# Kernel optimization log

Hardware: AMD Instinct MI355X
Metric: run time of the kernel (lower is better)

## Reference

```python
import jax, jax.numpy as jnp
import numpy as np

IN_H = IN_W = 128
OUT_H = OUT_W = 512
CHUNK = 65536  # = 256*256, same chunk size as the torch while-loop
EPS = 1e-6


def _conv3(x, w, b):
    y = jax.lax.conv_general_dilated(x, w, (1, 1), ((1, 1), (1, 1)),
                                     dimension_numbers=('NCHW', 'OIHW', 'NCHW'))
    return y + b[None, :, None, None]


def _centers(n):
    # torch.arange(-1,1,2/n)+1/n  ==  cell centers in (-1,1)
    return (jnp.arange(n, dtype=jnp.float32) + 0.5) * (2.0 / n) - 1.0


def setup_inputs() -> dict:
    key = jax.random.key(0)
    ks = iter(jax.random.split(key, 40))
    rnd = lambda shape, s: jax.random.normal(next(ks), shape, jnp.float32) * s
    inp = {
        'x': jax.random.uniform(next(ks), (1, 3, IN_H, IN_W), jnp.float32),
        'output_size': jnp.array([OUT_H, OUT_W], dtype=jnp.int32),
        # EDSR encoder params
        'head_w': rnd((64, 3, 3, 3), 0.05), 'head_b': rnd((64,), 0.01),
        'rb_w': rnd((16, 2, 64, 64, 3, 3), 0.02), 'rb_b': rnd((16, 2, 64), 0.01),
        'tail_w': rnd((64, 64, 3, 3), 0.02), 'tail_b': rnd((64,), 0.01),
        # MLP 580 -> 256 -> 256 -> 256 -> 256 -> 3
        'mw0': rnd((580, 256), 0.04), 'mb0': rnd((256,), 0.01),
        'mw1': rnd((256, 256), 0.06), 'mb1': rnd((256,), 0.01),
        'mw2': rnd((256, 256), 0.06), 'mb2': rnd((256,), 0.01),
        'mw3': rnd((256, 256), 0.06), 'mb3': rnd((256,), 0.01),
        'mw4': rnd((256, 3), 0.06), 'mb4': rnd((3,), 0.01),
    }
    return inp


def reference(x, output_size, head_w, head_b, rb_w, rb_b, tail_w, tail_b,
              mw0, mb0, mw1, mb1, mw2, mb2, mw3, mb3, mw4, mb4):
    # ---- EDSR encoder (head conv + 16 resblocks + tail conv, residual) ----
    h0 = _conv3(x, head_w, head_b)

    def block(h, wb):
        w0, b0, w1, b1 = wb
        return h + _conv3(jax.nn.relu(_conv3(h, w0, b0)), w1, b1), None

    hb, _ = jax.lax.scan(block, h0, (rb_w[:, 0], rb_b[:, 0], rb_w[:, 1], rb_b[:, 1]))
    feat64 = h0 + _conv3(hb, tail_w, tail_b)  # [1,64,H,W]
    B, C, H, W = feat64.shape

    # im2col 3x3 pad 1 -> channel order (c, kh, kw), matching torch im2col.view
    p = jnp.pad(feat64, ((0, 0), (0, 0), (1, 1), (1, 1)))
    feat = jnp.stack([p[:, :, i:i + H, j:j + W]
                      for i in range(3) for j in range(3)],
                     axis=2).reshape(B, C * 9, H, W)  # [1,576,H,W]

    # normalized cell-center coordinate map of the feature grid: [2,H,W], (h,w)
    fg = jnp.stack(jnp.meshgrid(_centers(H), _centers(W), indexing='ij'))

    ws = (mw0, mw1, mw2, mw3, mw4)
    bs = (mb0, mb1, mb2, mb3, mb4)

    def mlp(t):
        for w, b in zip(ws[:-1], bs[:-1]):
            t = jax.nn.relu(t @ w + b)
        return t @ ws[-1] + bs[-1]

    dh, dw = 1.0 / H, 1.0 / W
    hw = jnp.array([H, W], jnp.float32)
    q_cell = jnp.array([2.0 * H / OUT_H, 2.0 * W / OUT_W], jnp.float32)
    fimg = feat[0]  # [576,H,W]

    def sample(img, gh, gw):
        # torch grid_sampler nearest, align_corners=False, round-half-to-even
        iy = jnp.clip(jnp.round(((gh + 1.0) * H - 1.0) * 0.5), 0, H - 1).astype(jnp.int32)
        ix = jnp.clip(jnp.round(((gw + 1.0) * W - 1.0) * 0.5), 0, W - 1).astype(jnp.int32)
        return img[:, iy, ix].T  # [P, C]

    def query_chunk(s_grid):  # [P,2] = (h,w) normalized coords
        preds, areas = [], []
        for r in (0, 1):
            for c in (0, 1):
                gh = jnp.clip(s_grid[:, 0] + (2.0 * r - 1.0) * dh, -1 + EPS, 1 - EPS)
                gw = jnp.clip(s_grid[:, 1] + (2.0 * c - 1.0) * dw, -1 + EPS, 1 - EPS)
                q_feat = sample(fimg, gh, gw)            # [P,576]
                q_grid = sample(fg, gh, gw)              # [P,2]
                rel = (s_grid - q_grid) * hw             # [P,2]
                inp = jnp.concatenate(
                    [q_feat, rel, jnp.broadcast_to(q_cell, rel.shape)], axis=-1)
                preds.append(mlp(inp))                   # [P,3]
                areas.append(jnp.abs(rel[:, 0] * rel[:, 1]))
        tot = areas[0] + areas[1] + areas[2] + areas[3] + 1e-9
        # LIIF local ensembling with swapped (diagonal) areas
        num = (preds[0] * areas[3][:, None] + preds[1] * areas[2][:, None]
               + preds[2] * areas[1][:, None] + preds[3] * areas[0][:, None])
        return num / tot[:, None]

    grid = jnp.stack(jnp.meshgrid(_centers(OUT_H), _centers(OUT_W), indexing='ij'),
                     axis=-1).reshape(-1, 2)             # [n,2]
    chunks = grid.reshape(-1, CHUNK, 2)                  # [nc,CHUNK,2]
    ys = jax.lax.map(query_chunk, chunks)                # [nc,CHUNK,3]
    y = ys.reshape(OUT_H, OUT_W, 3).transpose(2, 0, 1)[None]  # [1,3,OH,OW]
    return jnp.clip(y, 0.0, 1.0)
```

## Files before the change

### kernel.cpp

```cpp
#include <hip/hip_runtime.h>
#include <hip/hip_fp16.h>

typedef __attribute__((ext_vector_type(8))) _Float16 half8;
typedef __attribute__((ext_vector_type(4))) _Float16 half4;
typedef __attribute__((ext_vector_type(4))) float float4v;

#define NPIX 16384

__device__ inline half8 h8zero() {
    half8 z = {(_Float16)0, (_Float16)0, (_Float16)0, (_Float16)0,
               (_Float16)0, (_Float16)0, (_Float16)0, (_Float16)0};
    return z;
}

__global__ void pack_all(const float* __restrict__ rb_w, const float* __restrict__ tail_w,
                         const float* __restrict__ mw0, const float* __restrict__ mw1,
                         const float* __restrict__ mw2, const float* __restrict__ mw3,
                         const float* __restrict__ mw4, const float* __restrict__ mb0,
                         _Float16* __restrict__ pwc, _Float16* __restrict__ pw0,
                         _Float16* __restrict__ pwm, float* __restrict__ b0p) {
    int idx = blockIdx.x * 256 + threadIdx.x;
    if (idx < 1216512) {
        int ci = idx / 36864;
        int e  = idx % 36864;
        int j = e & 7, ln = (e >> 3) & 63, kcnt = e >> 9;
        int kc = kcnt % 18, ntc = kcnt / 18;
        int k = kc * 32 + (ln >> 4) * 8 + j;
        int nn = ntc * 16 + (ln & 15);
        int ij = k >> 6, c = k & 63;
        const float* src = (ci < 32) ? (rb_w + ci * 36864) : tail_w;
        pwc[idx] = (_Float16)src[(nn * 64 + c) * 9 + ij];
        return;
    }
    idx -= 1216512;
    if (idx < 147456) {
        int j = idx & 7, ln = (idx >> 3) & 63, kcnt = idx >> 9;
        int kc = kcnt % 18, ntc = kcnt / 18;
        int k = kc * 32 + (ln >> 4) * 8 + j;
        int nn = ntc * 16 + (ln & 15);
        int ij = k >> 6, c = k & 63;
        pw0[idx] = (_Float16)mw0[(c * 9 + ij) * 256 + nn];
        return;
    }
    idx -= 147456;
    if (idx < 200704) {
        if (idx < 196608) {
            int l = idx / 65536;
            int e = idx % 65536;
            int j = e & 7, ln = (e >> 3) & 63, kcnt = e >> 9;
            int kc = kcnt & 7, ntc = kcnt >> 3;
            int k = kc * 32 + (ln >> 4) * 8 + j;
            int nn = ntc * 16 + (ln & 15);
            const float* w = (l == 0) ? mw1 : ((l == 1) ? mw2 : mw3);
            pwm[idx] = (_Float16)w[k * 256 + nn];
        } else {
            int e = idx - 196608;
            int j = e & 7, ln = (e >> 3) & 63, kc = e >> 9;
            int k = kc * 32 + (ln >> 4) * 8 + j;
            int nn = ln & 15;
            pwm[idx] = (nn < 3) ? (_Float16)mw4[k * 3 + nn] : (_Float16)0.0f;
        }
        return;
    }
    idx -= 200704;
    if (idx < 256)
        b0p[idx] = mb0[idx] + 0.5f * (mw0[578 * 256 + idx] + mw0[579 * 256 + idx]);
}

__global__ void head_conv(const float* __restrict__ x, const float* __restrict__ w,
                          const float* __restrict__ b, _Float16* __restrict__ h0) {
    int idx = blockIdx.x * 256 + threadIdx.x;
    int o = idx & 63, p = idx >> 6;
    int py = p >> 7, px = p & 127;
    float acc = b[o];
    #pragma unroll
    for (int c = 0; c < 3; ++c)
        #pragma unroll
        for (int i = 0; i < 3; ++i)
            #pragma unroll
            for (int jj = 0; jj < 3; ++jj) {
                int y = py + i - 1, xx = px + jj - 1;
                if (y >= 0 && y < 128 && xx >= 0 && xx < 128)
                    acc += x[c * 16384 + y * 128 + xx] * w[((o * 3 + c) * 3 + i) * 3 + jj];
            }
    h0[idx] = (_Float16)acc;
}

#define LDS_STRIDE 72

template <int DH, int DW, int SW, int SOFF, int RES>
__device__ __forceinline__ void conv_stage(
    const _Float16* __restrict__ src, _Float16* __restrict__ dst, _Float16* __restrict__ INb,
    const _Float16* __restrict__ pw, const float* __restrict__ bias,
    int q, int r, int nb, int gy0, int gx0, _Float16* __restrict__ gout)
{
    half8 B[18];
    #pragma unroll
    for (int kc = 0; kc < 18; ++kc)
        B[kc] = *(const half8*)(pw + ((((nb >> 4) * 18 + kc) * 64 + (q << 4) + r) << 3));
    float bv = bias[nb + r];
    constexpr int NPXc = DH * DW;
    constexpr int NT = (NPXc + 15) >> 4;
    #pragma unroll 1
    for (int tl = 0; tl < NT; ++tl) {
        int pa = tl * 16 + r;
        int ca = pa < NPXc ? pa : NPXc - 1;
        int my = ca / DW, mx = ca % DW;
        float4v acc = {0.f, 0.f, 0.f, 0.f};
        #pragma unroll
        for (int kc = 0; kc < 18; ++kc) {
            int ij = kc >> 1;
            int di = ij / 3 - 1;
            int dj = ij % 3 - 1;
            int cb = ((kc & 1) << 5) + (q << 3);
            int sp = (my + 1 + di + SOFF) * SW + (mx + 1 + dj + SOFF);
            half8 a = *(const half8*)(src + sp * LDS_STRIDE + cb);
            acc = __builtin_amdgcn_mfma_f32_16x16x32_f16(a, B[kc], acc, 0, 0, 0);
        }
        #pragma unroll
        for (int reg = 0; reg < 4; ++reg) {
            int pc = tl * 16 + (q << 2) + reg;
            if (pc >= NPXc) continue;
            int dy = pc / DW, dx = pc % DW;
            int gy = gy0 + dy, gx = gx0 + dx;
            bool valid = (gy >= 0 && gy < 128 && gx >= 0 && gx < 128);
            if (RES == 0) {
                float v = fmaxf(acc[reg] + bv, 0.f);
                dst[pc * LDS_STRIDE + nb + r] = valid ? (_Float16)v : (_Float16)0.0f;
            } else if (RES == 1) {
                int sl = ((dy + 2) * 16 + dx + 2) * LDS_STRIDE + nb + r;
                float v = acc[reg] + bv + (float)INb[sl];
                INb[sl] = valid ? (_Float16)v : (_Float16)0.0f;
            } else {
                int sl = ((dy + 4) * 16 + dx + 4) * LDS_STRIDE + nb + r;
                float v = acc[reg] + bv + (float)INb[sl];
                gout[(((gy << 7) + gx) << 6) + nb + r] = (_Float16)v;
            }
        }
    }
}

__global__ __launch_bounds__(256, 3)
void rb_pair(const _Float16* __restrict__ img, const _Float16* __restrict__ pw,
             const float* __restrict__ bias, _Float16* __restrict__ out) {
    __shared__ _Float16 IN[192 * LDS_STRIDE];
    __shared__ _Float16 MID[140 * LDS_STRIDE];
    int t = threadIdx.x;
    int wave = t >> 6, lane = t & 63, q = lane >> 4, r = lane & 15;
    int tr = blockIdx.x >> 4, tc = blockIdx.x & 15;
    int ty0 = tr << 2, tx0 = tc << 3;
    int nb = wave << 4;

    #pragma unroll
    for (int i = 0; i < 6; ++i) {
        int idx = t + i * 256;
        int px = idx >> 3, c = idx & 7;
        int iy = px >> 4, ix = px & 15;
        int gy = ty0 - 4 + iy, gx = tx0 - 4 + ix;
        half8 v = h8zero();
        if (gy >= 0 && gy < 128 && gx >= 0 && gx < 128)
            v = *(const half8*)(img + (((gy << 7) + gx) << 6) + (c << 3));
        *(half8*)(IN + px * LDS_STRIDE + (c << 3)) = v;
    }
    __syncthreads();

    conv_stage<10, 14, 16, 0, 0>(IN, MID, IN, pw, bias, q, r, nb, ty0 - 3, tx0 - 3, nullptr);
    __syncthreads();
    conv_stage<8, 12, 14, 0, 1>(MID, nullptr, IN, pw + 36864, bias + 64, q, r, nb,
                                ty0 - 2, tx0 - 2, nullptr);
    __syncthreads();
    conv_stage<6, 10, 16, 2, 0>(IN, MID, IN, pw + 2 * 36864, bias + 128, q, r, nb,
                                ty0 - 1, tx0 - 1, nullptr);
    __syncthreads();
    conv_stage<4, 8, 10, 0, 2>(MID, nullptr, IN, pw + 3 * 36864, bias + 192, q, r, nb,
                               ty0, tx0, out);
}

template <int NTOT, int MTPER, bool RELU, bool RES, bool F32OUT>
__global__ __launch_bounds__(256, 2)
void conv_mfma_r(const _Float16* __restrict__ img, const _Float16* __restrict__ pw,
                 const float* __restrict__ bias, const _Float16* res,
                 _Float16* outh, float* outf) {
    int wave = threadIdx.x >> 6, lane = threadIdx.x & 63;
    int q = lane >> 4, r = lane & 15;
    int nt, mt0;
    if constexpr (NTOT == 4) {
        nt = wave;
        mt0 = blockIdx.x * MTPER;
    } else {
        nt = (blockIdx.x & 3) * 4 + wave;
        mt0 = (blockIdx.x >> 2) * MTPER;
    }
    half8 B[18];
    #pragma unroll
    for (int kc = 0; kc < 18; ++kc)
        B[kc] = *(const half8*)(pw + (((nt * 18 + kc) * 64 + lane) << 3));
    int n = nt * 16 + r;
    float bv = bias[n];
    #pragma unroll
    for (int mi = 0; mi < MTPER; ++mi) {
        int mt = mt0 + mi;
        int p0 = mt * 16;
        int py = p0 >> 7;
        int pxl = (p0 & 127) + r;
        float4v acc = {0.f, 0.f, 0.f, 0.f};
        #pragma unroll
        for (int kc = 0; kc < 18; ++kc) {
            int ij = kc >> 1;
            int di = ij / 3 - 1;
            int dj = ij % 3 - 1;
            int cb = ((kc & 1) << 5) + (q << 3);
            int yy = py + di, xx = pxl + dj;
            half8 a = h8zero();
            if (yy >= 0 && yy < 128 && xx >= 0 && xx < 128)
                a = *(const half8*)(img + (((yy << 7) + xx) << 6) + cb);
            acc = __builtin_amdgcn_mfma_f32_16x16x32_f16(a, B[kc], acc, 0, 0, 0);
        }
        #pragma unroll
        for (int reg = 0; reg < 4; ++reg) {
            int p = p0 + (q << 2) + reg;
            float v = acc[reg] + bv;
            if (RES) v += (float)res[p * (NTOT * 16) + n];
            if (RELU) v = fmaxf(v, 0.f);
            if (F32OUT) outf[p * (NTOT * 16) + n] = v;
            else        outh[p * (NTOT * 16) + n] = (_Float16)v;
        }
    }
}

__global__ __launch_bounds__(256, 3)
void mlp_kernel(const float* __restrict__ apre, const float* __restrict__ mw0,
                const float* __restrict__ mb1, const float* __restrict__ mb2,
                const float* __restrict__ mb3, const float* __restrict__ mb4,
                const _Float16* __restrict__ pwm, const _Float16* __restrict__ pw4,
                float* __restrict__ out) {
    __shared__ _Float16 act[16384];
    __shared__ float sArea[64], sRelH[64], sRelW[64];
    __shared__ int sCell[64];
    __shared__ float sWh[256], sWw[256];

    int t = threadIdx.x;
    int bid = blockIdx.x;
    int logical = (bid & 7) * 2048 + (bid >> 3);
    int p0 = logical << 4;

    if (t < 64) {
        int lp = t >> 2, rc = t & 3;
        int p = p0 + lp;
        int oh = p >> 9, ow = p & 511;
        float sh = (oh + 0.5f) * (2.0f / 512.0f) - 1.0f;
        float sw = (ow + 0.5f) * (2.0f / 512.0f) - 1.0f;
        float gh = sh + (((rc >> 1) != 0) ? (1.0f / 128.0f) : (-1.0f / 128.0f));
        float gw = sw + (((rc & 1) != 0) ? (1.0f / 128.0f) : (-1.0f / 128.0f));
        const float lim = 1.0f - 1e-6f;
        gh = fminf(fmaxf(gh, -lim), lim);
        gw = fminf(fmaxf(gw, -lim), lim);
        int iy = (int)rintf(((gh + 1.0f) * 128.0f - 1.0f) * 0.5f);
        int ix = (int)rintf(((gw + 1.0f) * 128.0f - 1.0f) * 0.5f);
        iy = iy < 0 ? 0 : (iy > 127 ? 127 : iy);
        ix = ix < 0 ? 0 : (ix > 127 ? 127 : ix);
        float cy = (iy + 0.5f) * (2.0f / 128.0f) - 1.0f;
        float cx = (ix + 0.5f) * (2.0f / 128.0f) - 1.0f;
        float rh = (sh - cy) * 128.0f;
        float rw = (sw - cx) * 128.0f;
        sCell[t] = (iy << 7) + ix;
        sRelH[t] = rh; sRelW[t] = rw;
        sArea[t] = fabsf(rh * rw);
    }
    sWh[t] = mw0[576 * 256 + t];
    sWw[t] = mw0[577 * 256 + t];
    __syncthreads();

    {
        int s = t >> 2, fb = (t & 3) << 6;
        float rh = sRelH[s], rw = sRelW[s];
        const float* ap = apre + ((size_t)sCell[s] << 8) + fb;
        int shi = s >> 4, slo = s & 15;
        #pragma unroll
        for (int n = 0; n < 64; n += 4) {
            int f = fb + n;
            float4v ld = *(const float4v*)(ap + n);
            half4 hv;
            #pragma unroll
            for (int kk = 0; kk < 4; ++kk) {
                float v = ld[kk] + rh * sWh[f + kk] + rw * sWw[f + kk];
                hv[kk] = (_Float16)fmaxf(v, 0.0f);
            }
            *(half4*)(act + ((((shi << 3) + (f >> 5)) * 64
                              + (((f >> 3) & 3) << 4) + slo) << 3) + (f & 7)) = hv;
        }
    }
    __syncthreads();

    int wave = t >> 6, lane = t & 63, q = lane >> 4, r = lane & 15;

    float4v acc[4][4];
    #pragma unroll 1
    for (int l = 0; l < 3; ++l) {
        #pragma unroll
        for (int mti = 0; mti < 4; ++mti)
            #pragma unroll
            for (int nts = 0; nts < 4; ++nts)
                acc[mti][nts] = (float4v){0.f, 0.f, 0.f, 0.f};
        const _Float16* pw = pwm + l * 65536;
        for (int kc = 0; kc < 8; ++kc) {
            half8 A[4], Bf[4];
            #pragma unroll
            for (int mti = 0; mti < 4; ++mti)
                A[mti] = *(const half8*)(pw + ((((wave * 4 + mti) * 8 + kc) * 64 + lane) << 3));
            #pragma unroll
            for (int nts = 0; nts < 4; ++nts)
                Bf[nts] = *(const half8*)(act + ((((nts << 3) + kc) * 64 + lane) << 3));
            #pragma unroll
            for (int mti = 0; mti < 4; ++mti)
                #pragma unroll
                for (int nts = 0; nts < 4; ++nts)
                    acc[mti][nts] = __builtin_amdgcn_mfma_f32_16x16x32_f16(
                        A[mti], Bf[nts], acc[mti][nts], 0, 0, 0);
        }
        const float* mb = (l == 0) ? mb1 : ((l == 1) ? mb2 : mb3);
        float4v bv[4];
        #pragma unroll
        for (int mti = 0; mti < 4; ++mti)
            bv[mti] = *(const float4v*)(mb + (wave << 6) + mti * 16 + (q << 2));
        __syncthreads();
        #pragma unroll
        for (int mti = 0; mti < 4; ++mti)
            #pragma unroll
            for (int nts = 0; nts < 4; ++nts) {
                int base = ((((nts << 3) + (wave << 1) + (mti >> 1)) * 64
                             + (((mti & 1) * 2 + (q >> 1)) << 4) + r) << 3) + ((q & 1) << 2);
                half4 hv;
                #pragma unroll
                for (int reg = 0; reg < 4; ++reg)
                    hv[reg] = (_Float16)fmaxf(acc[mti][nts][reg] + bv[mti][reg], 0.0f);
                *(half4*)(act + base) = hv;
            }
        __syncthreads();
    }

    float4v af = {0.f, 0.f, 0.f, 0.f};
    #pragma unroll
    for (int kc = 0; kc < 8; ++kc) {
        half8 A = *(const half8*)(pw4 + ((kc * 64 + lane) << 3));
        half8 Bf = *(const half8*)(act + ((((wave << 3) + kc) * 64 + lane) << 3));
        af = __builtin_amdgcn_mfma_f32_16x16x32_f16(A, Bf, af, 0, 0, 0);
    }
    int s = (wave << 4) + r;
    int lp = s >> 2, rc = s & 3;
    float ar = sArea[(lp << 2) + (3 - rc)];
    float c0 = (af[0] + mb4[0]) * ar;
    float c1 = (af[1] + mb4[1]) * ar;
    float c2 = (af[2] + mb4[2]) * ar;
    c0 += __shfl_xor(c0, 1); c1 += __shfl_xor(c1, 1); c2 += __shfl_xor(c2, 1);
    float at = ar + __shfl_xor(ar, 1);
    c0 += __shfl_xor(c0, 2); c1 += __shfl_xor(c1, 2); c2 += __shfl_xor(c2, 2);
    at += __shfl_xor(at, 2);
    if (q == 0 && rc == 0) {
        float inv = 1.0f / (at + 1e-9f);
        out[p0 + lp]          = fminf(fmaxf(c0 * inv, 0.0f), 1.0f);
        out[262144 + p0 + lp] = fminf(fmaxf(c1 * inv, 0.0f), 1.0f);
        out[524288 + p0 + lp] = fminf(fmaxf(c2 * inv, 0.0f), 1.0f);
    }
}

extern "C" void kernel_launch(void* const* d_in, const int* in_sizes, int n_in,
                              void* d_out, int out_size, void* d_ws, size_t ws_size,
                              hipStream_t stream) {
    (void)in_sizes; (void)n_in; (void)out_size; (void)ws_size;
    const float* x      = (const float*)d_in[0];
    const float* head_w = (const float*)d_in[2];
    const float* head_b = (const float*)d_in[3];
    const float* rb_w   = (const float*)d_in[4];
    const float* rb_b   = (const float*)d_in[5];
    const float* tail_w = (const float*)d_in[6];
    const float* tail_b = (const float*)d_in[7];
    const float* mw0    = (const float*)d_in[8];
    const float* mb0    = (const float*)d_in[9];
    const float* mw1    = (const float*)d_in[10];
    const float* mb1    = (const float*)d_in[11];
    const float* mw2    = (const float*)d_in[12];
    const float* mb2    = (const float*)d_in[13];
    const float* mw3    = (const float*)d_in[14];
    const float* mb3    = (const float*)d_in[15];
    const float* mw4    = (const float*)d_in[16];
    const float* mb4    = (const float*)d_in[17];
    float* out = (float*)d_out;

    char* w = (char*)d_ws;
    auto take = [&](size_t n) { char* p = w; w += (n + 255) & ~(size_t)255; return p; };
    _Float16* pwc  = (_Float16*)take(33u * 36864u * 2u);
    _Float16* pw0  = (_Float16*)take(147456u * 2u);
    _Float16* pwm  = (_Float16*)take(200704u * 2u);
    float*    b0p  = (float*)take(256u * 4u);
    _Float16* h0   = (_Float16*)take((size_t)NPIX * 64u * 2u);
    _Float16* hbuf = (_Float16*)take((size_t)NPIX * 64u * 2u);
    _Float16* tbuf = (_Float16*)take((size_t)NPIX * 64u * 2u);
    _Float16* feat = (_Float16*)take((size_t)NPIX * 64u * 2u);
    float*    apre = (float*)take((size_t)NPIX * 256u * 4u);

    pack_all<<<6113, 256, 0, stream>>>(rb_w, tail_w, mw0, mw1, mw2, mw3, mw4, mb0,
                                       pwc, pw0, pwm, b0p);
    head_conv<<<4096, 256, 0, stream>>>(x, head_w, head_b, h0);

    const _Float16* cur = h0;
    for (int p = 0; p < 8; ++p) {
        _Float16* dst = (p & 1) ? tbuf : hbuf;
        rb_pair<<<512, 256, 0, stream>>>(cur, pwc + 4 * p * 36864, rb_b + p * 256, dst);
        cur = dst;
    }
    conv_mfma_r<4, 2, false, true, false><<<512, 256, 0, stream>>>(
        cur, pwc + 32 * 36864, tail_b, h0, feat, nullptr);
    conv_mfma_r<16, 4, false, false, true><<<1024, 256, 0, stream>>>(
        feat, pw0, b0p, nullptr, nullptr, apre);

    mlp_kernel<<<16384, 256, 0, stream>>>(apre, mw0, mb1, mb2, mb3, mb4,
                                          pwm, pwm + 196608, out);
}
```

Before: 807.7 us.

## Transpose MLP MFMA operand roles, fold head conv into pack kernel, raise occupancy

Swaps the MFMA operand roles in the MLP kernel so activations become the A operand (samples as rows) and weights the B operand. This changes the LDS activation layout so the first-layer store is a single half8 write per chunk. The final layer's ensemble reduction now runs per lane without cross-lane shuffles. The head convolution is merged into the weight-packing kernel to save one launch, and the MLP launch bounds rise from 3 to 4 blocks per CU. The inter-layer writeback now uses scalar fp16 LDS stores instead of half4 stores, and the higher occupancy target may force register spills.

```diff
diff --git a/kernel.cpp b/kernel.cpp
--- a/kernel.cpp
+++ b/kernel.cpp
@@ -17,8 +17,11 @@
                          const float* __restrict__ mw0, const float* __restrict__ mw1,
                          const float* __restrict__ mw2, const float* __restrict__ mw3,
                          const float* __restrict__ mw4, const float* __restrict__ mb0,
+                         const float* __restrict__ x, const float* __restrict__ head_w,
+                         const float* __restrict__ head_b,
                          _Float16* __restrict__ pwc, _Float16* __restrict__ pw0,
-                         _Float16* __restrict__ pwm, float* __restrict__ b0p) {
+                         _Float16* __restrict__ pwm, float* __restrict__ b0p,
+                         _Float16* __restrict__ h0) {
     int idx = blockIdx.x * 256 + threadIdx.x;
     if (idx < 1216512) {
         int ci = idx / 36864;
@@ -63,27 +66,28 @@
         return;
     }
     idx -= 200704;
-    if (idx < 256)
+    if (idx < 256) {
         b0p[idx] = mb0[idx] + 0.5f * (mw0[578 * 256 + idx] + mw0[579 * 256 + idx]);
-}
-
-__global__ void head_conv(const float* __restrict__ x, const float* __restrict__ w,
-                          const float* __restrict__ b, _Float16* __restrict__ h0) {
-    int idx = blockIdx.x * 256 + threadIdx.x;
-    int o = idx & 63, p = idx >> 6;
-    int py = p >> 7, px = p & 127;
-    float acc = b[o];
-    #pragma unroll
-    for (int c = 0; c < 3; ++c)
-        #pragma unroll
-        for (int i = 0; i < 3; ++i)
-            #pragma unroll
-            for (int jj = 0; jj < 3; ++jj) {
-                int y = py + i - 1, xx = px + jj - 1;
-                if (y >= 0 && y < 128 && xx >= 0 && xx < 128)
-                    acc += x[c * 16384 + y * 128 + xx] * w[((o * 3 + c) * 3 + i) * 3 + jj];
-            }
-    h0[idx] = (_Float16)acc;
+        return;
+    }
+    idx -= 256;
+    if (idx < NPIX * 64) {
+        int o = idx & 63, p = idx >> 6;
+        int py = p >> 7, px = p & 127;
+        float acc = head_b[o];
+        #pragma unroll
+        for (int c = 0; c < 3; ++c)
+            #pragma unroll
+            for (int i = 0; i < 3; ++i)
+                #pragma unroll
+                for (int jj = 0; jj < 3; ++jj) {
+                    int y = py + i - 1, xx = px + jj - 1;
+                    if (y >= 0 && y < 128 && xx >= 0 && xx < 128)
+                        acc += x[c * 16384 + y * 128 + xx]
+                             * head_w[((o * 3 + c) * 3 + i) * 3 + jj];
+                }
+        h0[idx] = (_Float16)acc;
+    }
 }
 
 #define LDS_STRIDE 72
@@ -228,7 +232,7 @@
     }
 }
 
-__global__ __launch_bounds__(256, 3)
+__global__ __launch_bounds__(256, 4)
 void mlp_kernel(const float* __restrict__ apre, const float* __restrict__ mw0,
                 const float* __restrict__ mb1, const float* __restrict__ mb2,
                 const float* __restrict__ mb3, const float* __restrict__ mb4,
@@ -271,70 +275,75 @@
     sWw[t] = mw0[577 * 256 + t];
     __syncthreads();
 
+    int wave = t >> 6, lane = t & 63, q = lane >> 4, r = lane & 15;
+
     {
-        int s = t >> 2, fb = (t & 3) << 6;
+        int s = (wave << 4) + r;
         float rh = sRelH[s], rw = sRelW[s];
-        const float* ap = apre + ((size_t)sCell[s] << 8) + fb;
-        int shi = s >> 4, slo = s & 15;
-        #pragma unroll
-        for (int n = 0; n < 64; n += 4) {
-            int f = fb + n;
-            float4v ld = *(const float4v*)(ap + n);
-            half4 hv;
+        const float* ap = apre + ((size_t)sCell[s] << 8) + (q << 3);
+        #pragma unroll
+        for (int j = 0; j < 8; ++j) {
+            int f0 = (j << 5) + (q << 3);
+            float4v lo = *(const float4v*)(ap + (j << 5));
+            float4v hi = *(const float4v*)(ap + (j << 5) + 4);
+            half8 hv;
             #pragma unroll
             for (int kk = 0; kk < 4; ++kk) {
-                float v = ld[kk] + rh * sWh[f + kk] + rw * sWw[f + kk];
+                float v = lo[kk] + rh * sWh[f0 + kk] + rw * sWw[f0 + kk];
                 hv[kk] = (_Float16)fmaxf(v, 0.0f);
             }
-            *(half4*)(act + ((((shi << 3) + (f >> 5)) * 64
-                              + (((f >> 3) & 3) << 4) + slo) << 3) + (f & 7)) = hv;
-        }
-    }
-    __syncthreads();
-
-    int wave = t >> 6, lane = t & 63, q = lane >> 4, r = lane & 15;
+            #pragma unroll
+            for (int kk = 0; kk < 4; ++kk) {
+                float v = hi[kk] + rh * sWh[f0 + 4 + kk] + rw * sWw[f0 + 4 + kk];
+                hv[4 + kk] = (_Float16)fmaxf(v, 0.0f);
+            }
+            *(half8*)(act + ((((wave << 3) + j) * 64 + lane) << 3)) = hv;
+        }
+    }
+    __syncthreads();
 
     float4v acc[4][4];
     #pragma unroll 1
     for (int l = 0; l < 3; ++l) {
         #pragma unroll
-        for (int mti = 0; mti < 4; ++mti)
-            #pragma unroll
-            for (int nts = 0; nts < 4; ++nts)
-                acc[mti][nts] = (float4v){0.f, 0.f, 0.f, 0.f};
+        for (int mt = 0; mt < 4; ++mt)
+            #pragma unroll
+            for (int nt = 0; nt < 4; ++nt)
+                acc[mt][nt] = (float4v){0.f, 0.f, 0.f, 0.f};
         const _Float16* pw = pwm + l * 65536;
         for (int kc = 0; kc < 8; ++kc) {
-            half8 A[4], Bf[4];
-            #pragma unroll
-            for (int mti = 0; mti < 4; ++mti)
-                A[mti] = *(const half8*)(pw + ((((wave * 4 + mti) * 8 + kc) * 64 + lane) << 3));
-            #pragma unroll
-            for (int nts = 0; nts < 4; ++nts)
-                Bf[nts] = *(const half8*)(act + ((((nts << 3) + kc) * 64 + lane) << 3));
-            #pragma unroll
-            for (int mti = 0; mti < 4; ++mti)
+            half8 A[4], B[4];
+            #pragma unroll
+            for (int mt = 0; mt < 4; ++mt)
+                A[mt] = *(const half8*)(act + (((mt * 8 + kc) * 64 + lane) << 3));
+            #pragma unroll
+            for (int nt = 0; nt < 4; ++nt)
+                B[nt] = *(const half8*)(pw + ((((wave * 4 + nt) * 8 + kc) * 64 + lane) << 3));
+            #pragma unroll
+            for (int mt = 0; mt < 4; ++mt)
                 #pragma unroll
-                for (int nts = 0; nts < 4; ++nts)
-                    acc[mti][nts] = __builtin_amdgcn_mfma_f32_16x16x32_f16(
-                        A[mti], Bf[nts], acc[mti][nts], 0, 0, 0);
+                for (int nt = 0; nt < 4; ++nt)
+                    acc[mt][nt] = __builtin_amdgcn_mfma_f32_16x16x32_f16(
+                        A[mt], B[nt], acc[mt][nt], 0, 0, 0);
         }
         const float* mb = (l == 0) ? mb1 : ((l == 1) ? mb2 : mb3);
-        float4v bv[4];
-        #pragma unroll
-        for (int mti = 0; mti < 4; ++mti)
-            bv[mti] = *(const float4v*)(mb + (wave << 6) + mti * 16 + (q << 2));
+        float bv[4];
+        #pragma unroll
+        for (int nt = 0; nt < 4; ++nt)
+            bv[nt] = mb[(wave << 6) + nt * 16 + r];
         __syncthreads();
         #pragma unroll
-        for (int mti = 0; mti < 4; ++mti)
-            #pragma unroll
-            for (int nts = 0; nts < 4; ++nts) {
-                int base = ((((nts << 3) + (wave << 1) + (mti >> 1)) * 64
-                             + (((mti & 1) * 2 + (q >> 1)) << 4) + r) << 3) + ((q & 1) << 2);
-                half4 hv;
+        for (int mt = 0; mt < 4; ++mt)
+            #pragma unroll
+            for (int nt = 0; nt < 4; ++nt) {
+                int kcp = (wave << 1) + (nt >> 1);
+                int qp  = ((nt & 1) << 1) + (r >> 3);
+                int base = ((mt * 8 + kcp) * 64 + qp * 16 + (q << 2)) * 8 + (r & 7);
                 #pragma unroll
-                for (int reg = 0; reg < 4; ++reg)
-                    hv[reg] = (_Float16)fmaxf(acc[mti][nts][reg] + bv[mti][reg], 0.0f);
-                *(half4*)(act + base) = hv;
+                for (int reg = 0; reg < 4; ++reg) {
+                    float v = fmaxf(acc[mt][nt][reg] + bv[nt], 0.0f);
+                    act[base + reg * 8] = (_Float16)v;
+                }
             }
         __syncthreads();
     }
@@ -342,25 +351,21 @@
     float4v af = {0.f, 0.f, 0.f, 0.f};
     #pragma unroll
     for (int kc = 0; kc < 8; ++kc) {
-        half8 A = *(const half8*)(pw4 + ((kc * 64 + lane) << 3));
-        half8 Bf = *(const half8*)(act + ((((wave << 3) + kc) * 64 + lane) << 3));
-        af = __builtin_amdgcn_mfma_f32_16x16x32_f16(A, Bf, af, 0, 0, 0);
-    }
-    int s = (wave << 4) + r;
-    int lp = s >> 2, rc = s & 3;
-    float ar = sArea[(lp << 2) + (3 - rc)];
-    float c0 = (af[0] + mb4[0]) * ar;
-    float c1 = (af[1] + mb4[1]) * ar;
-    float c2 = (af[2] + mb4[2]) * ar;
-    c0 += __shfl_xor(c0, 1); c1 += __shfl_xor(c1, 1); c2 += __shfl_xor(c2, 1);
-    float at = ar + __shfl_xor(ar, 1);
-    c0 += __shfl_xor(c0, 2); c1 += __shfl_xor(c1, 2); c2 += __shfl_xor(c2, 2);
-    at += __shfl_xor(at, 2);
-    if (q == 0 && rc == 0) {
-        float inv = 1.0f / (at + 1e-9f);
-        out[p0 + lp]          = fminf(fmaxf(c0 * inv, 0.0f), 1.0f);
-        out[262144 + p0 + lp] = fminf(fmaxf(c1 * inv, 0.0f), 1.0f);
-        out[524288 + p0 + lp] = fminf(fmaxf(c2 * inv, 0.0f), 1.0f);
+        half8 A = *(const half8*)(act + (((wave * 8 + kc) * 64 + lane) << 3));
+        half8 B = *(const half8*)(pw4 + ((kc * 64 + lane) << 3));
+        af = __builtin_amdgcn_mfma_f32_16x16x32_f16(A, B, af, 0, 0, 0);
+    }
+    if (r < 3) {
+        float b4 = mb4[r];
+        int lp = (wave << 2) + q;
+        float a0 = sArea[lp * 4 + 0], a1 = sArea[lp * 4 + 1];
+        float a2 = sArea[lp * 4 + 2], a3 = sArea[lp * 4 + 3];
+        float tot = a0 + a1 + a2 + a3 + 1e-9f;
+        float num = (af[0] + b4) * a3 + (af[1] + b4) * a2
+                  + (af[2] + b4) * a1 + (af[3] + b4) * a0;
+        float v = num / tot;
+        v = fminf(fmaxf(v, 0.0f), 1.0f);
+        out[r * 262144 + p0 + lp] = v;
     }
 }
 
@@ -399,9 +404,8 @@
     _Float16* feat = (_Float16*)take((size_t)NPIX * 64u * 2u);
     float*    apre = (float*)take((size_t)NPIX * 256u * 4u);
 
-    pack_all<<<6113, 256, 0, stream>>>(rb_w, tail_w, mw0, mw1, mw2, mw3, mw4, mb0,
-                                       pwc, pw0, pwm, b0p);
-    head_conv<<<4096, 256, 0, stream>>>(x, head_w, head_b, h0);
+    pack_all<<<10209, 256, 0, stream>>>(rb_w, tail_w, mw0, mw1, mw2, mw3, mw4, mb0,
+                                        x, head_w, head_b, pwc, pw0, pwm, b0p, h0);
 
     const _Float16* cur = h0;
     for (int p = 0; p < 8; ++p) {
```

After: 759.8 us. 1.06x faster.

## Fuse head conv into pack kernel, raise MLP occupancy, restructure layer-0 activation writes

Applied to the files above, without the earlier changes.

Merges the head convolution into the weight-packing kernel so one launch is removed. Raises the mlp_kernel launch bound from 3 to 4 blocks per CU, which may force register spills. Rewrites the first-layer activation staging so each lane builds a full half8 fragment and stores it contiguously into LDS in MFMA layout, replacing the scattered half4 stores.

```diff
diff --git a/kernel.cpp b/kernel.cpp
--- a/kernel.cpp
+++ b/kernel.cpp
@@ -17,8 +17,11 @@
                          const float* __restrict__ mw0, const float* __restrict__ mw1,
                          const float* __restrict__ mw2, const float* __restrict__ mw3,
                          const float* __restrict__ mw4, const float* __restrict__ mb0,
+                         const float* __restrict__ x, const float* __restrict__ head_w,
+                         const float* __restrict__ head_b,
                          _Float16* __restrict__ pwc, _Float16* __restrict__ pw0,
-                         _Float16* __restrict__ pwm, float* __restrict__ b0p) {
+                         _Float16* __restrict__ pwm, float* __restrict__ b0p,
+                         _Float16* __restrict__ h0) {
     int idx = blockIdx.x * 256 + threadIdx.x;
     if (idx < 1216512) {
         int ci = idx / 36864;
@@ -63,27 +66,28 @@
         return;
     }
     idx -= 200704;
-    if (idx < 256)
+    if (idx < 256) {
         b0p[idx] = mb0[idx] + 0.5f * (mw0[578 * 256 + idx] + mw0[579 * 256 + idx]);
-}
-
-__global__ void head_conv(const float* __restrict__ x, const float* __restrict__ w,
-                          const float* __restrict__ b, _Float16* __restrict__ h0) {
-    int idx = blockIdx.x * 256 + threadIdx.x;
-    int o = idx & 63, p = idx >> 6;
-    int py = p >> 7, px = p & 127;
-    float acc = b[o];
-    #pragma unroll
-    for (int c = 0; c < 3; ++c)
-        #pragma unroll
-        for (int i = 0; i < 3; ++i)
-            #pragma unroll
-            for (int jj = 0; jj < 3; ++jj) {
-                int y = py + i - 1, xx = px + jj - 1;
-                if (y >= 0 && y < 128 && xx >= 0 && xx < 128)
-                    acc += x[c * 16384 + y * 128 + xx] * w[((o * 3 + c) * 3 + i) * 3 + jj];
-            }
-    h0[idx] = (_Float16)acc;
+        return;
+    }
+    idx -= 256;
+    if (idx < NPIX * 64) {
+        int o = idx & 63, p = idx >> 6;
+        int py = p >> 7, px = p & 127;
+        float acc = head_b[o];
+        #pragma unroll
+        for (int c = 0; c < 3; ++c)
+            #pragma unroll
+            for (int i = 0; i < 3; ++i)
+                #pragma unroll
+                for (int jj = 0; jj < 3; ++jj) {
+                    int y = py + i - 1, xx = px + jj - 1;
+                    if (y >= 0 && y < 128 && xx >= 0 && xx < 128)
+                        acc += x[c * 16384 + y * 128 + xx]
+                             * head_w[((o * 3 + c) * 3 + i) * 3 + jj];
+                }
+        h0[idx] = (_Float16)acc;
+    }
 }
 
 #define LDS_STRIDE 72
@@ -228,7 +232,7 @@
     }
 }
 
-__global__ __launch_bounds__(256, 3)
+__global__ __launch_bounds__(256, 4)
 void mlp_kernel(const float* __restrict__ apre, const float* __restrict__ mw0,
                 const float* __restrict__ mb1, const float* __restrict__ mb2,
                 const float* __restrict__ mb3, const float* __restrict__ mb4,
@@ -271,28 +275,32 @@
     sWw[t] = mw0[577 * 256 + t];
     __syncthreads();
 
+    int wave = t >> 6, lane = t & 63, q = lane >> 4, r = lane & 15;
+
     {
-        int s = t >> 2, fb = (t & 3) << 6;
+        int s = (wave << 4) + r;
         float rh = sRelH[s], rw = sRelW[s];
-        const float* ap = apre + ((size_t)sCell[s] << 8) + fb;
-        int shi = s >> 4, slo = s & 15;
-        #pragma unroll
-        for (int n = 0; n < 64; n += 4) {
-            int f = fb + n;
-            float4v ld = *(const float4v*)(ap + n);
-            half4 hv;
+        const float* ap = apre + ((size_t)sCell[s] << 8) + (q << 3);
+        #pragma unroll
+        for (int j = 0; j < 8; ++j) {
+            int f0 = (j << 5) + (q << 3);
+            float4v lo = *(const float4v*)(ap + (j << 5));
+            float4v hi = *(const float4v*)(ap + (j << 5) + 4);
+            half8 hv;
             #pragma unroll
             for (int kk = 0; kk < 4; ++kk) {
-                float v = ld[kk] + rh * sWh[f + kk] + rw * sWw[f + kk];
+                float v = lo[kk] + rh * sWh[f0 + kk] + rw * sWw[f0 + kk];
                 hv[kk] = (_Float16)fmaxf(v, 0.0f);
             }
-            *(half4*)(act + ((((shi << 3) + (f >> 5)) * 64
-                              + (((f >> 3) & 3) << 4) + slo) << 3) + (f & 7)) = hv;
-        }
-    }
-    __syncthreads();
-
-    int wave = t >> 6, lane = t & 63, q = lane >> 4, r = lane & 15;
+            #pragma unroll
+            for (int kk = 0; kk < 4; ++kk) {
+                float v = hi[kk] + rh * sWh[f0 + 4 + kk] + rw * sWw[f0 + 4 + kk];
+                hv[4 + kk] = (_Float16)fmaxf(v, 0.0f);
+            }
+            *(half8*)(act + ((((wave << 3) + j) * 64 + lane) << 3)) = hv;
+        }
+    }
+    __syncthreads();
 
     float4v acc[4][4];
     #pragma unroll 1
@@ -399,9 +407,8 @@
     _Float16* feat = (_Float16*)take((size_t)NPIX * 64u * 2u);
     float*    apre = (float*)take((size_t)NPIX * 256u * 4u);
 
-    pack_all<<<6113, 256, 0, stream>>>(rb_w, tail_w, mw0, mw1, mw2, mw3, mw4, mb0,
-                                       pwc, pw0, pwm, b0p);
-    head_conv<<<4096, 256, 0, stream>>>(x, head_w, head_b, h0);
+    pack_all<<<10209, 256, 0, stream>>>(rb_w, tail_w, mw0, mw1, mw2, mw3, mw4, mb0,
+                                        x, head_w, head_b, pwc, pw0, pwm, b0p, h0);
 
     const _Float16* cur = h0;
     for (int p = 0; p < 8; ++p) {
```

Result: slower. 938.6 us (+16.2%).
